# Performance work log

Measured on AMD Instinct MI355X. Metric: run time of the kernel, lower is better.

The kernel has to match this reference:

```python
import jax, jax.numpy as jnp
import numpy as np

N = 250000   # nodes
E = 500000   # edges
D = 128      # embed_dim
L = 4        # num_layer - 1 conv layers
G = 10000    # graphs in batch
OUT = 128    # output_dim
AV = 120     # atom vocab per feature
BV = 6       # bond vocab per feature
EPS_GN = 1e-6


def setup_inputs() -> dict:
    key = jax.random.key(0)
    ks = jax.random.split(key, 12)
    s = 0.02
    f32 = jnp.float32
    inp = {}
    inp["nfeat"] = jax.random.randint(ks[0], (N, 9), 0, AV)
    inp["efeat"] = jax.random.randint(ks[1], (E, 3), 0, BV)
    inp["src"] = jax.random.randint(ks[2], (E,), 0, N)
    inp["dst"] = jax.random.randint(ks[3], (E,), 0, N)
    inp["graph_ids"] = jnp.arange(N, dtype=jnp.int32) // (N // G)  # 25 nodes/graph
    # learned params
    inp["atom_emb"] = jax.random.normal(ks[4], (9, AV, D), f32) * s
    inp["bond_emb"] = jax.random.normal(ks[5], (L, 3, BV, D), f32) * s
    inp["W1"] = jax.random.normal(ks[6], (L, D, 2 * D), f32) * s
    inp["b1"] = jnp.zeros((L, 2 * D), f32)
    inp["gn1_w"] = jnp.ones((L, 2 * D), f32)
    inp["gn1_b"] = jnp.zeros((L, 2 * D), f32)
    inp["gn1_ms"] = jnp.ones((L, 2 * D), f32)  # GraphNorm mean_scale
    inp["W2"] = jax.random.normal(ks[7], (L, 2 * D, D), f32) * s
    inp["b2"] = jnp.zeros((L, D), f32)
    inp["gn2_w"] = jnp.ones((L, D), f32)
    inp["gn2_b"] = jnp.zeros((L, D), f32)
    inp["gn2_ms"] = jnp.ones((L, D), f32)
    inp["Wp"] = jax.random.normal(ks[8], (D, OUT), f32) * s
    inp["bp"] = jnp.zeros((OUT,), f32)
    return inp


def graph_norm(x, gids, counts, w, b, ms):
    # GraphNorm: x - mean_scale * per-graph mean, / per-graph std, affine
    mean = jax.ops.segment_sum(x, gids, num_segments=G) / counts  # [G, D]
    sub = x - mean[gids] * ms
    var = jax.ops.segment_sum(sub * sub, gids, num_segments=G) / counts
    std = jnp.sqrt(var + EPS_GN)
    return w * sub / std[gids] + b


def reference(nfeat, efeat, src, dst, graph_ids, atom_emb, bond_emb,
              W1, b1, gn1_w, gn1_b, gn1_ms, W2, b2, gn2_w, gn2_b, gn2_ms,
              Wp, bp):
    counts = jax.ops.segment_sum(jnp.ones((N, 1), jnp.float32), graph_ids,
                                 num_segments=G)  # [G,1]
    # AtomEncoder: sum of 9 per-feature embeddings
    h = jnp.sum(atom_emb[jnp.arange(9)[None, :], nfeat], axis=1)  # [N, D]
    eps = jnp.float32(0.0)  # GIN eps buffer, init 0, not learned
    for l in range(L):
        x = h
        # BondEncoder for layer l
        he = jnp.sum(bond_emb[l][jnp.arange(3)[None, :], efeat], axis=1)  # [E, D]
        m = h[src] + he                                   # copy_u + edge add
        agg = jax.ops.segment_sum(m, dst, num_segments=N)  # sum reduce
        rst = (agg + (1.0 + eps) * h) @ W1[l] + b1[l]
        rst = graph_norm(rst, graph_ids, counts, gn1_w[l], gn1_b[l], gn1_ms[l])
        rst = jax.nn.relu(rst) @ W2[l] + b2[l]
        rst = graph_norm(rst, graph_ids, counts, gn2_w[l], gn2_b[l], gn2_ms[l])
        if l != L - 1:
            rst = jax.nn.relu(rst)  # activation for all but last conv layer
        h = rst + x  # residual
    # mean pooling over graphs
    g = jax.ops.segment_sum(h, graph_ids, num_segments=G) / counts  # [G, D]
    # dropout is identity in eval mode
    return g @ Wp + bp
```

## Files before the change

### kernel.cpp

```cpp
#include <hip/hip_runtime.h>
#include <hip/hip_bf16.h>
#include <stdint.h>

#define N_NODES 250000
#define N_EDGES 500000
#define DIM     128
#define D2      256
#define NLAYER  4
#define NGRAPH  10000
#define NPG     25
#define ATOMV   120
#define BONDV   6

typedef __attribute__((ext_vector_type(4))) float f32x4;
typedef __attribute__((ext_vector_type(8))) short bf16x8;

__device__ __forceinline__ unsigned short bf16c(float x) {
    union { __hip_bfloat16 b; unsigned short u; } v;
    v.b = __float2bfloat16(x);
    return v.u;
}
__device__ __forceinline__ float bf16_up(unsigned short b) {
    union { float f; unsigned u; } v; v.u = (unsigned)b << 16;
    return v.f;
}
__device__ __forceinline__ f32x4 up4(ushort4 v) {
    f32x4 r;
    r[0] = bf16_up(v.x); r[1] = bf16_up(v.y);
    r[2] = bf16_up(v.z); r[3] = bf16_up(v.w);
    return r;
}

template<int CTRL>
__device__ __forceinline__ float dppadd(float x) {
    return x + __builtin_bit_cast(float,
        __builtin_amdgcn_update_dpp(0, __builtin_bit_cast(int, x),
                                    CTRL, 0xF, 0xF, true));
}
template<int CTRL>
__device__ __forceinline__ void red_step(f32x4& s0, f32x4& q0, f32x4& s1, f32x4& q1) {
#pragma unroll
    for (int j = 0; j < 4; ++j) {
        s0[j] = dppadd<CTRL>(s0[j]);
        q0[j] = dppadd<CTRL>(q0[j]);
        s1[j] = dppadd<CTRL>(s1[j]);
        q1[j] = dppadd<CTRL>(q1[j]);
    }
}
__device__ __forceinline__ void red16(f32x4& s0, f32x4& q0, f32x4& s1, f32x4& q1) {
    red_step<0xB1>(s0, q0, s1, q1);
    red_step<0x4E>(s0, q0, s1, q1);
    red_step<0x124>(s0, q0, s1, q1);
    red_step<0x128>(s0, q0, s1, q1);
}

__global__ void k_atom(const int* __restrict__ nfeat, const float* __restrict__ aemb,
                       unsigned short* __restrict__ h) {
    int t = blockIdx.x * 256 + threadIdx.x;
    int n = t >> 5;
    if (n >= N_NODES) return;
    int q = (t & 31) * 4;
    f32x4 acc = {0.f, 0.f, 0.f, 0.f};
#pragma unroll
    for (int f = 0; f < 9; ++f) {
        int v = nfeat[n * 9 + f];
        acc += *(const f32x4*)(aemb + ((size_t)(f * ATOMV + v) * DIM + q));
    }
    ushort4 hv;
    hv.x = bf16c(acc[0]); hv.y = bf16c(acc[1]);
    hv.z = bf16c(acc[2]); hv.w = bf16c(acc[3]);
    *(ushort4*)(h + (size_t)n * DIM + q) = hv;
}

__global__ void k_zero_i(int* __restrict__ p, int n) {
    int i = blockIdx.x * 256 + threadIdx.x;
    if (i < n) p[i] = 0;
}
__global__ void k_hist(const int* __restrict__ dst, int* __restrict__ deg) {
    int e = blockIdx.x * 256 + threadIdx.x;
    if (e < N_EDGES) atomicAdd(&deg[dst[e]], 1);
}
__global__ void k_scan_block(const int* __restrict__ deg, int* __restrict__ rp,
                             int* __restrict__ bsum) {
    __shared__ int s[1024];
    int x = threadIdx.x;
    int i = blockIdx.x * 1024 + x;
    s[x] = (i < N_NODES) ? deg[i] : 0;
    __syncthreads();
#pragma unroll
    for (int off = 1; off < 1024; off <<= 1) {
        int tv = (x >= off) ? s[x - off] : 0;
        __syncthreads();
        s[x] += tv;
        __syncthreads();
    }
    if (i < N_NODES) rp[i + 1] = s[x];
    if (x == 1023) bsum[blockIdx.x] = s[1023];
}
__global__ void k_scan_sums(int* __restrict__ bsum, int nb) {
    __shared__ int s[256];
    int x = threadIdx.x;
    s[x] = (x < nb) ? bsum[x] : 0;
    __syncthreads();
#pragma unroll
    for (int off = 1; off < 256; off <<= 1) {
        int tv = (x >= off) ? s[x - off] : 0;
        __syncthreads();
        s[x] += tv;
        __syncthreads();
    }
    if (x < nb) bsum[x] = s[x];
}
__global__ void k_scan_add(int* __restrict__ rp, const int* __restrict__ bsum) {
    int i = blockIdx.x * 1024 + threadIdx.x;
    if (blockIdx.x > 0 && i < N_NODES) rp[i + 1] += bsum[blockIdx.x - 1];
    if (blockIdx.x == 0 && threadIdx.x == 0) rp[0] = 0;
}
__global__ void k_copy_i(const int* __restrict__ a, int* __restrict__ b, int n) {
    int i = blockIdx.x * 256 + threadIdx.x;
    if (i < n) b[i] = a[i];
}
__global__ void k_fill(const int* __restrict__ dst, int* __restrict__ cur,
                       int* __restrict__ elist) {
    int e = blockIdx.x * 256 + threadIdx.x;
    if (e < N_EDGES) {
        int p = atomicAdd(&cur[dst[e]], 1);
        elist[p] = e;
    }
}

__global__ void k_gather(const unsigned short* __restrict__ h, const int* __restrict__ efeat,
                         const int* __restrict__ src, const int* __restrict__ rp,
                         const int* __restrict__ elist, const float* __restrict__ bemb,
                         unsigned short* __restrict__ xh) {
    int t = blockIdx.x * 256 + threadIdx.x;
    int n = t >> 5;
    if (n >= N_NODES) return;
    int q = (t & 31) * 4;
    f32x4 acc = up4(*(const ushort4*)(h + (size_t)n * DIM + q));
    int e0 = rp[n], e1 = rp[n + 1];
    for (int p = e0; p < e1; ++p) {
        int e = elist[p];
        int s = src[e];
        f32x4 m = up4(*(const ushort4*)(h + (size_t)s * DIM + q));
#pragma unroll
        for (int f = 0; f < 3; ++f) {
            int v = efeat[e * 3 + f];
            m += *(const f32x4*)(bemb + (size_t)(f * BONDV + v) * DIM + q);
        }
        acc += m;
    }
    ushort4 hv;
    hv.x = bf16c(acc[0]); hv.y = bf16c(acc[1]);
    hv.z = bf16c(acc[2]); hv.w = bf16c(acc[3]);
    *(ushort4*)(xh + (size_t)n * DIM + q) = hv;
}

__global__ void k_prepw(const float* __restrict__ W1, const float* __restrict__ W2,
                        unsigned short* __restrict__ w1h, unsigned short* __restrict__ w2h) {
    int i = blockIdx.x * 256 + threadIdx.x;
    if (i >= NLAYER * DIM * D2) return;
    {
        int l = i / (DIM * D2), rem = i % (DIM * D2);
        int k = rem / D2, n = rem % D2;
        w1h[l * DIM * D2 + n * DIM + k] = bf16c(W1[i]);
    }
    {
        int l = i / (D2 * DIM), rem = i % (D2 * DIM);
        int k = rem / DIM, n = rem % DIM;
        w2h[l * D2 * DIM + n * D2 + k] = bf16c(W2[i]);
    }
}


__device__ __forceinline__ void gn1_store(
    f32x4 acc1[2][4],
    const float* __restrict__ b1g, const float* __restrict__ g1w,
    const float* __restrict__ g1b, const float* __restrict__ g1ms,
    int w, int l15, int lhi, int half, unsigned short* __restrict__ B)
{
#pragma unroll
    for (int mi = 0; mi < 2; ++mi) {
        const int chl = 32 * w + 16 * mi + 4 * lhi;
        const int chg = half * 128 + chl;
        f32x4 s0 = {}, q0 = {}, s1 = {}, q1 = {};
        {
            f32x4 v = acc1[mi][0]; s0 += v; q0 += v * v;
            v = acc1[mi][1];
            if (l15 < 9) { s0 += v; q0 += v * v; } else { s1 += v; q1 += v * v; }
            v = acc1[mi][2]; s1 += v; q1 += v * v;
            v = acc1[mi][3];
            if (l15 < 2) { s1 += v; q1 += v * v; }
        }
        red16(s0, q0, s1, q1);
        f32x4 b1v = *(const f32x4*)(b1g + chg);
        f32x4 msv = *(const f32x4*)(g1ms + chg);
        f32x4 wv  = *(const f32x4*)(g1w + chg);
        f32x4 bbv = *(const f32x4*)(g1b + chg);
        f32x4 mr0 = s0 * 0.04f, mr1 = s1 * 0.04f;
        f32x4 off0 = msv * (mr0 + b1v) - b1v;
        f32x4 off1 = msv * (mr1 + b1v) - b1v;
        f32x4 var0 = q0 * 0.04f - 2.f * off0 * mr0 + off0 * off0;
        f32x4 var1 = q1 * 0.04f - 2.f * off1 * mr1 + off1 * off1;
        f32x4 sc0, sc1;
#pragma unroll
        for (int j = 0; j < 4; ++j) {
            sc0[j] = wv[j] * rsqrtf(var0[j] + 1e-6f);
            sc1[j] = wv[j] * rsqrtf(var1[j] + 1e-6f);
        }
#pragma unroll
        for (int ni = 0; ni < 4; ++ni) {
            int nd = l15 + 16 * ni;
            bool gsel = (nd >= NPG);
            f32x4 off_ = gsel ? off1 : off0;
            f32x4 sc_  = gsel ? sc1 : sc0;
            f32x4 y = (acc1[mi][ni] - off_) * sc_ + bbv;
            ushort4 hv;
            unsigned short* hp = (unsigned short*)&hv;
#pragma unroll
            for (int j = 0; j < 4; ++j)
                hp[j] = bf16c(fmaxf(y[j], 0.f));
            int gp = ((chl >> 3) - 2 * nd) & 15;
            int ao = nd * 136 + gp * 8 + (chl & 7);
            *(ushort4*)&B[ao] = hv;
        }
    }
}

__device__ __forceinline__ void mm2_half(
    const unsigned short* __restrict__ B,
    const unsigned short* __restrict__ w2h,
    int w, int l15, int lhi, int half, f32x4 acc2[2][4])
{
#pragma unroll
    for (int ks = 0; ks < 4; ++ks) {
        const int kb = ks * 32 + lhi * 8;
        const int g = kb >> 3;
        bf16x8 x2[4];
#pragma unroll
        for (int ni = 0; ni < 4; ++ni) {
            int nd = l15 + 16 * ni;
            int gp = (g - 2 * nd) & 15;
            x2[ni] = *(const bf16x8*)&B[nd * 136 + gp * 8];
        }
#pragma unroll
        for (int mi = 0; mi < 2; ++mi) {
            const size_t wro = (size_t)(32 * w + 16 * mi + l15) * 256 + half * 128 + kb;
            bf16x8 wh = *(const bf16x8*)(w2h + wro);
#pragma unroll
            for (int ni = 0; ni < 4; ++ni)
                acc2[mi][ni] = __builtin_amdgcn_mfma_f32_16x16x32_bf16(wh, x2[ni], acc2[mi][ni], 0, 0, 0);
        }
    }
}

__global__ __launch_bounds__(256, 3) void k_layer(
    const unsigned short* __restrict__ xh_g,
    unsigned short* __restrict__ h,
    const unsigned short* __restrict__ w1h,
    const float* __restrict__ b1g,
    const float* __restrict__ g1w, const float* __restrict__ g1b, const float* __restrict__ g1ms,
    const unsigned short* __restrict__ w2h,
    const float* __restrict__ b2g,
    const float* __restrict__ g2w, const float* __restrict__ g2b, const float* __restrict__ g2ms,
    int do_relu)
{
    __shared__ unsigned short B0[64 * 136];
    __shared__ unsigned short B1[64 * 136];

    const int t = threadIdx.x;
    const int lane = t & 63;
    const int w = t >> 6;
    const int l15 = lane & 15, lhi = lane >> 4;
    const size_t row0 = (size_t)blockIdx.x * 50;

    int ndrow[4];
#pragma unroll
    for (int ni = 0; ni < 4; ++ni) {
        int nd = l15 + 16 * ni;
        ndrow[ni] = (nd < 50) ? nd : 49;
    }

    f32x4 a1h0[2][4] = {};
    f32x4 a1h1[2][4] = {};
#pragma unroll
    for (int ks = 0; ks < 4; ++ks) {
        const int kb = ks * 32 + lhi * 8;
        bf16x8 xv[4];
#pragma unroll
        for (int ni = 0; ni < 4; ++ni)
            xv[ni] = *(const bf16x8*)(xh_g + (row0 + ndrow[ni]) * DIM + kb);
#pragma unroll
        for (int mi = 0; mi < 2; ++mi) {
            const size_t wr0 = (size_t)(32 * w + 16 * mi + l15) * 128 + kb;
            const size_t wr1 = (size_t)(128 + 32 * w + 16 * mi + l15) * 128 + kb;
            bf16x8 wh0 = *(const bf16x8*)(w1h + wr0);
            bf16x8 wh1 = *(const bf16x8*)(w1h + wr1);
#pragma unroll
            for (int ni = 0; ni < 4; ++ni) {
                a1h0[mi][ni] = __builtin_amdgcn_mfma_f32_16x16x32_bf16(wh0, xv[ni], a1h0[mi][ni], 0, 0, 0);
                a1h1[mi][ni] = __builtin_amdgcn_mfma_f32_16x16x32_bf16(wh1, xv[ni], a1h1[mi][ni], 0, 0, 0);
            }
        }
    }

    gn1_store(a1h0, b1g, g1w, g1b, g1ms, w, l15, lhi, 0, B0);
    gn1_store(a1h1, b1g, g1w, g1b, g1ms, w, l15, lhi, 1, B1);
    __syncthreads();

    f32x4 acc2[2][4] = {};
    mm2_half(B0, w2h, w, l15, lhi, 0, acc2);
    mm2_half(B1, w2h, w, l15, lhi, 1, acc2);

#pragma unroll
    for (int mi = 0; mi < 2; ++mi) {
        const int chb = 32 * w + 16 * mi + 4 * lhi;
        f32x4 s0 = {}, q0 = {}, s1 = {}, q1 = {};
        {
            f32x4 v = acc2[mi][0]; s0 += v; q0 += v * v;
            v = acc2[mi][1];
            if (l15 < 9) { s0 += v; q0 += v * v; } else { s1 += v; q1 += v * v; }
            v = acc2[mi][2]; s1 += v; q1 += v * v;
            v = acc2[mi][3];
            if (l15 < 2) { s1 += v; q1 += v * v; }
        }
        red16(s0, q0, s1, q1);
        f32x4 b2v = *(const f32x4*)(b2g + chb);
        f32x4 msv = *(const f32x4*)(g2ms + chb);
        f32x4 wv  = *(const f32x4*)(g2w + chb);
        f32x4 bbv = *(const f32x4*)(g2b + chb);
        f32x4 mr0 = s0 * 0.04f, mr1 = s1 * 0.04f;
        f32x4 off0 = msv * (mr0 + b2v) - b2v;
        f32x4 off1 = msv * (mr1 + b2v) - b2v;
        f32x4 var0 = q0 * 0.04f - 2.f * off0 * mr0 + off0 * off0;
        f32x4 var1 = q1 * 0.04f - 2.f * off1 * mr1 + off1 * off1;
        f32x4 sc0, sc1;
#pragma unroll
        for (int j = 0; j < 4; ++j) {
            sc0[j] = wv[j] * rsqrtf(var0[j] + 1e-6f);
            sc1[j] = wv[j] * rsqrtf(var1[j] + 1e-6f);
        }
#pragma unroll
        for (int ni = 0; ni < 4; ++ni) {
            int nd = l15 + 16 * ni;
            if (nd < 50) {
                bool gsel = (nd >= NPG);
                f32x4 off_ = gsel ? off1 : off0;
                f32x4 sc_  = gsel ? sc1 : sc0;
                f32x4 y = (acc2[mi][ni] - off_) * sc_ + bbv;
                if (do_relu) {
#pragma unroll
                    for (int j = 0; j < 4; ++j) y[j] = fmaxf(y[j], 0.f);
                }
                unsigned short* hp = h + (row0 + nd) * DIM + chb;
                f32x4 hf = up4(*(const ushort4*)hp);
                f32x4 r = y + hf;
                ushort4 o;
                o.x = bf16c(r[0]); o.y = bf16c(r[1]);
                o.z = bf16c(r[2]); o.w = bf16c(r[3]);
                *(ushort4*)hp = o;
            }
        }
    }
}

__global__ void k_pool(const unsigned short* __restrict__ h, float* __restrict__ g) {
    int gi = blockIdx.x, c = threadIdx.x;
    const unsigned short* base = h + (size_t)gi * NPG * DIM + c;
    float s = 0.f;
#pragma unroll
    for (int i = 0; i < NPG; ++i) s += bf16_up(base[i * DIM]);
    g[(size_t)gi * DIM + c] = s * (1.f / NPG);
}

#define GPB 32
__global__ __launch_bounds__(256) void k_final(const float* __restrict__ g,
        const float* __restrict__ Wp, const float* __restrict__ bp,
        float* __restrict__ out) {
    __shared__ float Ws[DIM * DIM];
    __shared__ float gs[GPB][DIM];
    int t = threadIdx.x;
    int g0 = blockIdx.x * GPB;
    for (int i = t; i < DIM * DIM; i += 256) Ws[i] = Wp[i];
    for (int i = t; i < GPB * DIM; i += 256) {
        int gi = g0 + i / DIM;
        gs[i / DIM][i % DIM] = (gi < NGRAPH) ? g[(size_t)gi * DIM + (i % DIM)] : 0.f;
    }
    __syncthreads();
    int c = t & (DIM - 1);
    int half = t >> 7;
    float bv = bp[c];
    for (int gl = half; gl < GPB; gl += 2) {
        int gi = g0 + gl;
        if (gi >= NGRAPH) continue;
        float s = 0.f;
#pragma unroll 8
        for (int k = 0; k < DIM; ++k) s += gs[gl][k] * Ws[k * DIM + c];
        out[(size_t)gi * DIM + c] = s + bv;
    }
}

extern "C" void kernel_launch(void* const* d_in, const int* in_sizes, int n_in,
                              void* d_out, int out_size, void* d_ws, size_t ws_size,
                              hipStream_t stream) {
    const int*   nfeat    = (const int*)d_in[0];
    const int*   efeat    = (const int*)d_in[1];
    const int*   src      = (const int*)d_in[2];
    const int*   dst      = (const int*)d_in[3];
    const float* atom_emb = (const float*)d_in[5];
    const float* bond_emb = (const float*)d_in[6];
    const float* W1       = (const float*)d_in[7];
    const float* b1       = (const float*)d_in[8];
    const float* gn1_w    = (const float*)d_in[9];
    const float* gn1_b    = (const float*)d_in[10];
    const float* gn1_ms   = (const float*)d_in[11];
    const float* W2       = (const float*)d_in[12];
    const float* b2       = (const float*)d_in[13];
    const float* gn2_w    = (const float*)d_in[14];
    const float* gn2_b    = (const float*)d_in[15];
    const float* gn2_ms   = (const float*)d_in[16];
    const float* Wp       = (const float*)d_in[17];
    const float* bp       = (const float*)d_in[18];
    float* out = (float*)d_out;

    char* ws = (char*)d_ws;
    unsigned short* w1h = (unsigned short*)ws; ws += (size_t)NLAYER * DIM * D2 * 2;
    unsigned short* w2h = (unsigned short*)ws; ws += (size_t)NLAYER * D2 * DIM * 2;
    unsigned short* h  = (unsigned short*)ws; ws += (size_t)N_NODES * DIM * 2;
    unsigned short* xh = (unsigned short*)ws; ws += (size_t)N_NODES * DIM * 2;
    float* gbuf = (float*)ws; ws += (size_t)NGRAPH * DIM * 4;

    int* rp    = (int*)d_out;
    int* elist = rp + 262144;
    int* cur   = elist + 524288;
    int* deg   = cur;
    int* bsum  = cur + 262144;

    const int NB = (N_NODES + 1023) / 1024;

    k_prepw<<<(NLAYER * DIM * D2 + 255) / 256, 256, 0, stream>>>(W1, W2, w1h, w2h);
    k_atom<<<(N_NODES * 32) / 256, 256, 0, stream>>>(nfeat, atom_emb, h);

    k_zero_i<<<(N_NODES + 255) / 256, 256, 0, stream>>>(deg, N_NODES);
    k_hist<<<(N_EDGES + 255) / 256, 256, 0, stream>>>(dst, deg);
    k_scan_block<<<NB, 1024, 0, stream>>>(deg, rp, bsum);
    k_scan_sums<<<1, 256, 0, stream>>>(bsum, NB);
    k_scan_add<<<NB, 1024, 0, stream>>>(rp, bsum);
    k_copy_i<<<(N_NODES + 255) / 256, 256, 0, stream>>>(rp, cur, N_NODES);
    k_fill<<<(N_EDGES + 255) / 256, 256, 0, stream>>>(dst, cur, elist);

    for (int l = 0; l < NLAYER; ++l) {
        k_gather<<<(N_NODES * 32 + 255) / 256, 256, 0, stream>>>(
            h, efeat, src, rp, elist, bond_emb + (size_t)l * 3 * BONDV * DIM, xh);
        k_layer<<<NGRAPH / 2, 256, 0, stream>>>(
            xh, h,
            w1h + l * DIM * D2, b1 + l * D2,
            gn1_w + l * D2, gn1_b + l * D2, gn1_ms + l * D2,
            w2h + l * D2 * DIM, b2 + l * DIM,
            gn2_w + l * DIM, gn2_b + l * DIM, gn2_ms + l * DIM,
            (l != NLAYER - 1) ? 1 : 0);
    }
    k_pool<<<NGRAPH, DIM, 0, stream>>>(h, gbuf);
    k_final<<<(NGRAPH + GPB - 1) / GPB, 256, 0, stream>>>(gbuf, Wp, bp, out);
}
```

Baseline: 1.107 ms.

## Fuse neighbor gather into layer kernel with ping-pong node buffers

The separate edge-aggregation kernel is folded into the per-layer MLP/GraphNorm kernel. Each block gathers neighbor messages for its 50 nodes into a swizzled LDS tile and feeds the first GEMM from LDS. Because the gather reads other blocks' rows, h is now double-buffered (hA/hB). This drops the xh round trip through global memory and one launch per layer. In exchange it adds 17 KB more LDS per block, which may cut occupancy, and the irregular gather now runs inside the MFMA kernel.

```diff
diff --git a/kernel.cpp b/kernel.cpp
--- a/kernel.cpp
+++ b/kernel.cpp
@@ -127,33 +127,6 @@
         int p = atomicAdd(&cur[dst[e]], 1);
         elist[p] = e;
     }
-}
-
-__global__ void k_gather(const unsigned short* __restrict__ h, const int* __restrict__ efeat,
-                         const int* __restrict__ src, const int* __restrict__ rp,
-                         const int* __restrict__ elist, const float* __restrict__ bemb,
-                         unsigned short* __restrict__ xh) {
-    int t = blockIdx.x * 256 + threadIdx.x;
-    int n = t >> 5;
-    if (n >= N_NODES) return;
-    int q = (t & 31) * 4;
-    f32x4 acc = up4(*(const ushort4*)(h + (size_t)n * DIM + q));
-    int e0 = rp[n], e1 = rp[n + 1];
-    for (int p = e0; p < e1; ++p) {
-        int e = elist[p];
-        int s = src[e];
-        f32x4 m = up4(*(const ushort4*)(h + (size_t)s * DIM + q));
-#pragma unroll
-        for (int f = 0; f < 3; ++f) {
-            int v = efeat[e * 3 + f];
-            m += *(const f32x4*)(bemb + (size_t)(f * BONDV + v) * DIM + q);
-        }
-        acc += m;
-    }
-    ushort4 hv;
-    hv.x = bf16c(acc[0]); hv.y = bf16c(acc[1]);
-    hv.z = bf16c(acc[2]); hv.w = bf16c(acc[3]);
-    *(ushort4*)(xh + (size_t)n * DIM + q) = hv;
 }
 
 __global__ void k_prepw(const float* __restrict__ W1, const float* __restrict__ W2,
@@ -255,8 +228,11 @@
 }
 
 __global__ __launch_bounds__(256, 3) void k_layer(
-    const unsigned short* __restrict__ xh_g,
-    unsigned short* __restrict__ h,
+    const unsigned short* __restrict__ hin,
+    unsigned short* __restrict__ hout,
+    const int* __restrict__ efeat, const int* __restrict__ src,
+    const int* __restrict__ rp, const int* __restrict__ elist,
+    const float* __restrict__ bemb,
     const unsigned short* __restrict__ w1h,
     const float* __restrict__ b1g,
     const float* __restrict__ g1w, const float* __restrict__ g1b, const float* __restrict__ g1ms,
@@ -265,6 +241,7 @@
     const float* __restrict__ g2w, const float* __restrict__ g2b, const float* __restrict__ g2ms,
     int do_relu)
 {
+    __shared__ unsigned short X [64 * 136];
     __shared__ unsigned short B0[64 * 136];
     __shared__ unsigned short B1[64 * 136];
 
@@ -274,6 +251,30 @@
     const int l15 = lane & 15, lhi = lane >> 4;
     const size_t row0 = (size_t)blockIdx.x * 50;
 
+    for (int u = t; u < 1600; u += 256) {
+        int r = u >> 5, q = (u & 31) * 4;
+        size_t n = row0 + r;
+        f32x4 acc = up4(*(const ushort4*)(hin + n * DIM + q));
+        int e0 = rp[n], e1 = rp[n + 1];
+        for (int p = e0; p < e1; ++p) {
+            int e = elist[p];
+            int s = src[e];
+            f32x4 m = up4(*(const ushort4*)(hin + (size_t)s * DIM + q));
+#pragma unroll
+            for (int f = 0; f < 3; ++f) {
+                int v = efeat[e * 3 + f];
+                m += *(const f32x4*)(bemb + (size_t)(f * BONDV + v) * DIM + q);
+            }
+            acc += m;
+        }
+        ushort4 hv;
+        hv.x = bf16c(acc[0]); hv.y = bf16c(acc[1]);
+        hv.z = bf16c(acc[2]); hv.w = bf16c(acc[3]);
+        int gp = ((q >> 3) - 2 * r) & 15;
+        *(ushort4*)&X[r * 136 + gp * 8 + (q & 7)] = hv;
+    }
+    __syncthreads();
+
     int ndrow[4];
 #pragma unroll
     for (int ni = 0; ni < 4; ++ni) {
@@ -286,10 +287,13 @@
 #pragma unroll
     for (int ks = 0; ks < 4; ++ks) {
         const int kb = ks * 32 + lhi * 8;
+        const int g = kb >> 3;
         bf16x8 xv[4];
 #pragma unroll
-        for (int ni = 0; ni < 4; ++ni)
-            xv[ni] = *(const bf16x8*)(xh_g + (row0 + ndrow[ni]) * DIM + kb);
+        for (int ni = 0; ni < 4; ++ni) {
+            int gp = (g - 2 * ndrow[ni]) & 15;
+            xv[ni] = *(const bf16x8*)&X[ndrow[ni] * 136 + gp * 8];
+        }
 #pragma unroll
         for (int mi = 0; mi < 2; ++mi) {
             const size_t wr0 = (size_t)(32 * w + 16 * mi + l15) * 128 + kb;
@@ -352,13 +356,12 @@
 #pragma unroll
                     for (int j = 0; j < 4; ++j) y[j] = fmaxf(y[j], 0.f);
                 }
-                unsigned short* hp = h + (row0 + nd) * DIM + chb;
-                f32x4 hf = up4(*(const ushort4*)hp);
+                f32x4 hf = up4(*(const ushort4*)(hin + (row0 + nd) * DIM + chb));
                 f32x4 r = y + hf;
                 ushort4 o;
                 o.x = bf16c(r[0]); o.y = bf16c(r[1]);
                 o.z = bf16c(r[2]); o.w = bf16c(r[3]);
-                *(ushort4*)hp = o;
+                *(ushort4*)(hout + (row0 + nd) * DIM + chb) = o;
             }
         }
     }
@@ -426,8 +429,8 @@
     char* ws = (char*)d_ws;
     unsigned short* w1h = (unsigned short*)ws; ws += (size_t)NLAYER * DIM * D2 * 2;
     unsigned short* w2h = (unsigned short*)ws; ws += (size_t)NLAYER * D2 * DIM * 2;
-    unsigned short* h  = (unsigned short*)ws; ws += (size_t)N_NODES * DIM * 2;
-    unsigned short* xh = (unsigned short*)ws; ws += (size_t)N_NODES * DIM * 2;
+    unsigned short* hA = (unsigned short*)ws; ws += (size_t)N_NODES * DIM * 2;
+    unsigned short* hB = (unsigned short*)ws; ws += (size_t)N_NODES * DIM * 2;
     float* gbuf = (float*)ws; ws += (size_t)NGRAPH * DIM * 4;
 
     int* rp    = (int*)d_out;
@@ -439,7 +442,7 @@
     const int NB = (N_NODES + 1023) / 1024;
 
     k_prepw<<<(NLAYER * DIM * D2 + 255) / 256, 256, 0, stream>>>(W1, W2, w1h, w2h);
-    k_atom<<<(N_NODES * 32) / 256, 256, 0, stream>>>(nfeat, atom_emb, h);
+    k_atom<<<(N_NODES * 32) / 256, 256, 0, stream>>>(nfeat, atom_emb, hA);
 
     k_zero_i<<<(N_NODES + 255) / 256, 256, 0, stream>>>(deg, N_NODES);
     k_hist<<<(N_EDGES + 255) / 256, 256, 0, stream>>>(dst, deg);
@@ -450,16 +453,17 @@
     k_fill<<<(N_EDGES + 255) / 256, 256, 0, stream>>>(dst, cur, elist);
 
     for (int l = 0; l < NLAYER; ++l) {
-        k_gather<<<(N_NODES * 32 + 255) / 256, 256, 0, stream>>>(
-            h, efeat, src, rp, elist, bond_emb + (size_t)l * 3 * BONDV * DIM, xh);
+        const unsigned short* hin  = (l & 1) ? hB : hA;
+        unsigned short*       hout = (l & 1) ? hA : hB;
         k_layer<<<NGRAPH / 2, 256, 0, stream>>>(
-            xh, h,
+            hin, hout, efeat, src, rp, elist,
+            bond_emb + (size_t)l * 3 * BONDV * DIM,
             w1h + l * DIM * D2, b1 + l * D2,
             gn1_w + l * D2, gn1_b + l * D2, gn1_ms + l * D2,
             w2h + l * D2 * DIM, b2 + l * DIM,
             gn2_w + l * DIM, gn2_b + l * DIM, gn2_ms + l * DIM,
             (l != NLAYER - 1) ? 1 : 0);
     }
-    k_pool<<<NGRAPH, DIM, 0, stream>>>(h, gbuf);
+    k_pool<<<NGRAPH, DIM, 0, stream>>>(hA, gbuf);
     k_final<<<(NGRAPH + GPB - 1) / GPB, 256, 0, stream>>>(gbuf, Wp, bp, out);
 }
```

Result: slower. 1.343 ms (+21.3%).

## Pack src and bond code into CSR entries and precombine bond embeddings

Applied to the files above, without the earlier changes.

Precomputes a table of all 216 summed bond-embedding combinations per layer. Each CSR entry now packs the source index and bond code into one int, so the gather does one indexed load instead of elist, src and three efeat/bemb lookups per edge. The layer kernel also loads residual h values before the second matmul so their latency overlaps with compute. This cuts the scattered memory traffic in the gather and adds a small precompute kernel.

```diff
diff --git a/kernel.cpp b/kernel.cpp
--- a/kernel.cpp
+++ b/kernel.cpp
@@ -11,6 +11,7 @@
 #define NPG     25
 #define ATOMV   120
 #define BONDV   6
+#define NBCOMB  216
 
 typedef __attribute__((ext_vector_type(4))) float f32x4;
 typedef __attribute__((ext_vector_type(8))) short bf16x8;
@@ -72,6 +73,19 @@
     *(ushort4*)(h + (size_t)n * DIM + q) = hv;
 }
 
+__global__ void k_prepbs(const float* __restrict__ bemb, float* __restrict__ bS) {
+    int i = blockIdx.x * 256 + threadIdx.x;
+    if (i >= NLAYER * NBCOMB * DIM) return;
+    int l = i / (NBCOMB * DIM);
+    int rem = i % (NBCOMB * DIM);
+    int code = rem / DIM, c = rem % DIM;
+    int v0 = code / 36, v1 = (code / 6) % 6, v2 = code % 6;
+    const float* base = bemb + (size_t)l * 3 * BONDV * DIM;
+    bS[i] = base[0 * BONDV * DIM + v0 * DIM + c]
+          + base[1 * BONDV * DIM + v1 * DIM + c]
+          + base[2 * BONDV * DIM + v2 * DIM + c];
+}
+
 __global__ void k_zero_i(int* __restrict__ p, int n) {
     int i = blockIdx.x * 256 + threadIdx.x;
     if (i < n) p[i] = 0;
@@ -120,18 +134,20 @@
     int i = blockIdx.x * 256 + threadIdx.x;
     if (i < n) b[i] = a[i];
 }
-__global__ void k_fill(const int* __restrict__ dst, int* __restrict__ cur,
-                       int* __restrict__ elist) {
+__global__ void k_fill2(const int* __restrict__ dst, const int* __restrict__ src,
+                        const int* __restrict__ efeat,
+                        int* __restrict__ cur, int* __restrict__ csr) {
     int e = blockIdx.x * 256 + threadIdx.x;
     if (e < N_EDGES) {
+        int b = efeat[e * 3] * 36 + efeat[e * 3 + 1] * 6 + efeat[e * 3 + 2];
         int p = atomicAdd(&cur[dst[e]], 1);
-        elist[p] = e;
-    }
-}
-
-__global__ void k_gather(const unsigned short* __restrict__ h, const int* __restrict__ efeat,
-                         const int* __restrict__ src, const int* __restrict__ rp,
-                         const int* __restrict__ elist, const float* __restrict__ bemb,
+        csr[p] = (b << 18) | src[e];
+    }
+}
+
+__global__ void k_gather(const unsigned short* __restrict__ h,
+                         const int* __restrict__ rp, const int* __restrict__ csr,
+                         const float* __restrict__ bSl,
                          unsigned short* __restrict__ xh) {
     int t = blockIdx.x * 256 + threadIdx.x;
     int n = t >> 5;
@@ -140,15 +156,11 @@
     f32x4 acc = up4(*(const ushort4*)(h + (size_t)n * DIM + q));
     int e0 = rp[n], e1 = rp[n + 1];
     for (int p = e0; p < e1; ++p) {
-        int e = elist[p];
-        int s = src[e];
-        f32x4 m = up4(*(const ushort4*)(h + (size_t)s * DIM + q));
-#pragma unroll
-        for (int f = 0; f < 3; ++f) {
-            int v = efeat[e * 3 + f];
-            m += *(const f32x4*)(bemb + (size_t)(f * BONDV + v) * DIM + q);
-        }
-        acc += m;
+        int pk = csr[p];
+        int s = pk & 0x3FFFF;
+        int b = pk >> 18;
+        acc += up4(*(const ushort4*)(h + (size_t)s * DIM + q))
+             + *(const f32x4*)(bSl + (size_t)b * DIM + q);
     }
     ushort4 hv;
     hv.x = bf16c(acc[0]); hv.y = bf16c(acc[1]);
@@ -308,6 +320,15 @@
     gn1_store(a1h1, b1g, g1w, g1b, g1ms, w, l15, lhi, 1, B1);
     __syncthreads();
 
+    ushort4 hres[2][4];
+#pragma unroll
+    for (int mi = 0; mi < 2; ++mi) {
+        const int chb = 32 * w + 16 * mi + 4 * lhi;
+#pragma unroll
+        for (int ni = 0; ni < 4; ++ni)
+            hres[mi][ni] = *(const ushort4*)(h + (row0 + ndrow[ni]) * DIM + chb);
+    }
+
     f32x4 acc2[2][4] = {};
     mm2_half(B0, w2h, w, l15, lhi, 0, acc2);
     mm2_half(B1, w2h, w, l15, lhi, 1, acc2);
@@ -352,13 +373,12 @@
 #pragma unroll
                     for (int j = 0; j < 4; ++j) y[j] = fmaxf(y[j], 0.f);
                 }
-                unsigned short* hp = h + (row0 + nd) * DIM + chb;
-                f32x4 hf = up4(*(const ushort4*)hp);
+                f32x4 hf = up4(hres[mi][ni]);
                 f32x4 r = y + hf;
                 ushort4 o;
                 o.x = bf16c(r[0]); o.y = bf16c(r[1]);
                 o.z = bf16c(r[2]); o.w = bf16c(r[3]);
-                *(ushort4*)hp = o;
+                *(ushort4*)(h + (row0 + nd) * DIM + chb) = o;
             }
         }
     }
@@ -426,19 +446,21 @@
     char* ws = (char*)d_ws;
     unsigned short* w1h = (unsigned short*)ws; ws += (size_t)NLAYER * DIM * D2 * 2;
     unsigned short* w2h = (unsigned short*)ws; ws += (size_t)NLAYER * D2 * DIM * 2;
+    float* bS = (float*)ws; ws += (size_t)NLAYER * NBCOMB * DIM * 4;
     unsigned short* h  = (unsigned short*)ws; ws += (size_t)N_NODES * DIM * 2;
     unsigned short* xh = (unsigned short*)ws; ws += (size_t)N_NODES * DIM * 2;
     float* gbuf = (float*)ws; ws += (size_t)NGRAPH * DIM * 4;
 
-    int* rp    = (int*)d_out;
-    int* elist = rp + 262144;
-    int* cur   = elist + 524288;
-    int* deg   = cur;
-    int* bsum  = cur + 262144;
+    int* rp   = (int*)d_out;
+    int* cur  = rp + 262144;
+    int* deg  = cur;
+    int* csr  = cur + 262144;
+    int* bsum = csr + 524288;
 
     const int NB = (N_NODES + 1023) / 1024;
 
     k_prepw<<<(NLAYER * DIM * D2 + 255) / 256, 256, 0, stream>>>(W1, W2, w1h, w2h);
+    k_prepbs<<<(NLAYER * NBCOMB * DIM + 255) / 256, 256, 0, stream>>>(bond_emb, bS);
     k_atom<<<(N_NODES * 32) / 256, 256, 0, stream>>>(nfeat, atom_emb, h);
 
     k_zero_i<<<(N_NODES + 255) / 256, 256, 0, stream>>>(deg, N_NODES);
@@ -447,11 +469,11 @@
     k_scan_sums<<<1, 256, 0, stream>>>(bsum, NB);
     k_scan_add<<<NB, 1024, 0, stream>>>(rp, bsum);
     k_copy_i<<<(N_NODES + 255) / 256, 256, 0, stream>>>(rp, cur, N_NODES);
-    k_fill<<<(N_EDGES + 255) / 256, 256, 0, stream>>>(dst, cur, elist);
+    k_fill2<<<(N_EDGES + 255) / 256, 256, 0, stream>>>(dst, src, efeat, cur, csr);
 
     for (int l = 0; l < NLAYER; ++l) {
         k_gather<<<(N_NODES * 32 + 255) / 256, 256, 0, stream>>>(
-            h, efeat, src, rp, elist, bond_emb + (size_t)l * 3 * BONDV * DIM, xh);
+            h, rp, csr, bS + (size_t)l * NBCOMB * DIM, xh);
         k_layer<<<NGRAPH / 2, 256, 0, stream>>>(
             xh, h,
             w1h + l * DIM * D2, b1 + l * D2,
```

Measured after the change: 967.5 us (median of 3 runs). -12.6%, faster.
